# Performance work log

Hardware: AMD Instinct MI355X
Metric: run time of the kernel (lower is better)

Reference implementation:

```python
import jax, jax.numpy as jnp
import numpy as np

NGRAM = 3  # no_repeat_ngram_size from init_kwargs


def setup_inputs() -> dict:
    key = jax.random.key(0)
    k1, k2 = jax.random.split(key)
    B = 64 * 8          # bsz * beam_size
    L = 512             # step + 1 tokens generated so far
    V = 50257           # vocab
    tokens = jax.random.randint(k1, (B, L), 0, 50, dtype=jnp.int64)
    lprobs = jax.random.normal(k2, (B, V), dtype=jnp.float32)
    return {"tokens": tokens, "lprobs": lprobs, "bsz": 64, "beam_size": 8, "step": 511}


def _ngram_block(tokens, lprobs, step, n):
    """Vectorized equivalent of NGramRepeatBlock._no_repeat_ngram.

    For each row, the last n-1 tokens form the ngram prefix; any earlier
    position i in [0, step+2-n) whose (n-1)-gram matches it bans the token
    that followed it (tokens[i + n - 1]).
    """
    B, L = tokens.shape
    check = step + 2 - n  # number of start positions to check (static)
    if check <= 0:
        return lprobs
    # sliding (n-1)-gram windows at starts 0..check-1: (B, check, n-1)
    win_idx = jnp.arange(check)[:, None] + jnp.arange(n - 1)[None, :]
    windows = tokens[:, win_idx]
    prefix = tokens[:, L - (n - 1):]                    # (B, n-1) last n-1 tokens
    match = jnp.all(windows == prefix[:, None, :], -1)  # (B, check)
    banned_ids = tokens[:, n - 1: n - 1 + check]        # token following each window
    rows = jnp.arange(B)[:, None]
    banned = jnp.zeros(lprobs.shape, bool).at[rows, banned_ids].max(match)
    return jnp.where(banned, -jnp.inf, lprobs)


def reference(tokens, lprobs, bsz, beam_size, step):
    assert tokens.shape[0] == bsz * beam_size
    assert lprobs.shape[0] == bsz * beam_size
    return _ngram_block(tokens, lprobs, step, NGRAM)
```

## Files before the change

kernel.cpp:

```cpp
#include <hip/hip_runtime.h>

#define NGRAM 3
#define BAN_VALUE (-1.0e30f)

typedef float f32x4 __attribute__((ext_vector_type(4)));

#define UNROLL 4
#define TPB 256
#define BLK_F4 (TPB * UNROLL)

__global__ void __launch_bounds__(TPB)
copy_kernel(const float* __restrict__ in, float* __restrict__ out,
            long long n4) {
    const long long base = (long long)blockIdx.x * BLK_F4 + threadIdx.x;
    const f32x4* in4 = (const f32x4*)in;
    f32x4* out4 = (f32x4*)out;

    if (base + 3 * TPB < n4) {
        f32x4 v0 = __builtin_nontemporal_load(in4 + base);
        f32x4 v1 = __builtin_nontemporal_load(in4 + base + TPB);
        f32x4 v2 = __builtin_nontemporal_load(in4 + base + 2 * TPB);
        f32x4 v3 = __builtin_nontemporal_load(in4 + base + 3 * TPB);
        __builtin_nontemporal_store(v0, out4 + base);
        __builtin_nontemporal_store(v1, out4 + base + TPB);
        __builtin_nontemporal_store(v2, out4 + base + 2 * TPB);
        __builtin_nontemporal_store(v3, out4 + base + 3 * TPB);
    } else {
        for (int k = 0; k < UNROLL; ++k) {
            long long i = base + (long long)k * TPB;
            if (i < n4) {
                f32x4 v = __builtin_nontemporal_load(in4 + i);
                __builtin_nontemporal_store(v, out4 + i);
            }
        }
    }
}

__global__ void __launch_bounds__(TPB)
ban_kernel(const int* __restrict__ tokens, float* __restrict__ out,
           const int* __restrict__ step_p, int L, int V) {
    const int row = blockIdx.x;
    const int step = *step_p;
    const int check = step + 2 - NGRAM;
    if (check <= 0) return;

    const int* t = tokens + (long long)row * L;
    const int p0 = t[L - 2];
    const int p1 = t[L - 1];
    float* orow = out + (long long)row * V;

    for (int i = threadIdx.x; i < check; i += TPB) {
        if (t[i] == p0 && t[i + 1] == p1) {
            orow[t[i + 2]] = BAN_VALUE;
        }
    }
}

extern "C" void kernel_launch(void* const* d_in, const int* in_sizes, int n_in,
                              void* d_out, int out_size, void* d_ws, size_t ws_size,
                              hipStream_t stream) {
    const int*   tokens = (const int*)d_in[0];
    const float* lprobs = (const float*)d_in[1];
    const int*   step_p = (const int*)d_in[4];
    float*       out    = (float*)d_out;

    const int L = 512;
    const int B = in_sizes[0] / L;
    const int V = in_sizes[1] / B;
    const long long n = (long long)in_sizes[1];
    const long long n4 = n / 4;

    const int blocksA = (int)((n4 + BLK_F4 - 1) / BLK_F4);
    copy_kernel<<<blocksA, TPB, 0, stream>>>(lprobs, out, n4);

    ban_kernel<<<B, TPB, 0, stream>>>(tokens, out, step_p, L, V);
}
```

Before: 182.8 us.

## Fuse n-gram ban scatter into the streaming copy kernel

Merges the copy and ban kernels into one. Each copy block scans the token rows overlapping its slice, collects banned offsets in shared memory, and patches them into registers before the store. This removes the second launch and its scattered writes to global memory. In exchange, every block rescans full token rows (about 511 positions for one or two rows) and pays a per-block loop over the ban list, adding redundant token reads and compute to a bandwidth-bound copy.

```diff
diff --git a/kernel.cpp b/kernel.cpp
--- a/kernel.cpp
+++ b/kernel.cpp
@@ -8,51 +8,96 @@
 #define UNROLL 4
 #define TPB 256
 #define BLK_F4 (TPB * UNROLL)
+#define BLK_F  (BLK_F4 * 4)
+
+__device__ __forceinline__ f32x4 patch4(f32x4 v, int lane) {
+    v.x = (lane == 0) ? BAN_VALUE : v.x;
+    v.y = (lane == 1) ? BAN_VALUE : v.y;
+    v.z = (lane == 2) ? BAN_VALUE : v.z;
+    v.w = (lane == 3) ? BAN_VALUE : v.w;
+    return v;
+}
 
 __global__ void __launch_bounds__(TPB)
-copy_kernel(const float* __restrict__ in, float* __restrict__ out,
-            long long n4) {
-    const long long base = (long long)blockIdx.x * BLK_F4 + threadIdx.x;
+fused_kernel(const float* __restrict__ in, float* __restrict__ out,
+             const int* __restrict__ tokens, const int* __restrict__ step_p,
+             int L, int V, unsigned n_f)
+{
+    __shared__ int s_count;
+    __shared__ unsigned short s_list[1024];
+
+    const unsigned n4 = n_f >> 2;
+    const long long blk0 = (long long)blockIdx.x * BLK_F4;
+    const unsigned F0 = (unsigned)(blk0 * 4);
+    unsigned F1 = F0 + BLK_F; if (F1 > n_f) F1 = n_f;
+    const long long base = blk0 + threadIdx.x;
+    const bool blk_full = (blk0 + BLK_F4 <= (long long)n4);
+
+    if (threadIdx.x == 0) s_count = 0;
+    __syncthreads();
+
     const f32x4* in4 = (const f32x4*)in;
     f32x4* out4 = (f32x4*)out;
 
-    if (base + 3 * TPB < n4) {
-        f32x4 v0 = __builtin_nontemporal_load(in4 + base);
-        f32x4 v1 = __builtin_nontemporal_load(in4 + base + TPB);
-        f32x4 v2 = __builtin_nontemporal_load(in4 + base + 2 * TPB);
-        f32x4 v3 = __builtin_nontemporal_load(in4 + base + 3 * TPB);
+    f32x4 v0 = {}, v1 = {}, v2 = {}, v3 = {};
+    if (blk_full) {
+        v0 = __builtin_nontemporal_load(in4 + base);
+        v1 = __builtin_nontemporal_load(in4 + base + TPB);
+        v2 = __builtin_nontemporal_load(in4 + base + 2 * TPB);
+        v3 = __builtin_nontemporal_load(in4 + base + 3 * TPB);
+    } else {
+        if (base           < n4) v0 = __builtin_nontemporal_load(in4 + base);
+        if (base +     TPB < n4) v1 = __builtin_nontemporal_load(in4 + base + TPB);
+        if (base + 2 * TPB < n4) v2 = __builtin_nontemporal_load(in4 + base + 2 * TPB);
+        if (base + 3 * TPB < n4) v3 = __builtin_nontemporal_load(in4 + base + 3 * TPB);
+    }
+
+    const int step = *step_p;
+    const int check = step + 2 - NGRAM;
+    if (check > 0) {
+        const unsigned rlo = F0 / (unsigned)V;
+        const unsigned rhi = (F1 - 1) / (unsigned)V;
+        for (unsigned r = rlo; r <= rhi; ++r) {
+            const int* t = tokens + (long long)r * L;
+            const int p0 = t[L - 2];
+            const int p1 = t[L - 1];
+            for (int i = threadIdx.x; i < check; i += TPB) {
+                if (t[i] == p0 && t[i + 1] == p1) {
+                    const unsigned f = r * (unsigned)V + (unsigned)t[i + 2];
+                    if (f >= F0 && f < F1) {
+                        const int idx = atomicAdd(&s_count, 1);
+                        s_list[idx] = (unsigned short)(f - F0);
+                    }
+                }
+            }
+        }
+    }
+    __syncthreads();
+
+    const int cnt = s_count;
+    if (cnt > 0) {
+        const int tid = (int)threadIdx.x;
+        for (int j = 0; j < cnt; ++j) {
+            const int off  = (int)s_list[j];
+            const int q4   = off >> 2;
+            const int lane = off & 3;
+            if      (q4 == tid)            v0 = patch4(v0, lane);
+            else if (q4 == tid + TPB)      v1 = patch4(v1, lane);
+            else if (q4 == tid + 2 * TPB)  v2 = patch4(v2, lane);
+            else if (q4 == tid + 3 * TPB)  v3 = patch4(v3, lane);
+        }
+    }
+
+    if (blk_full) {
         __builtin_nontemporal_store(v0, out4 + base);
         __builtin_nontemporal_store(v1, out4 + base + TPB);
         __builtin_nontemporal_store(v2, out4 + base + 2 * TPB);
         __builtin_nontemporal_store(v3, out4 + base + 3 * TPB);
     } else {
-        for (int k = 0; k < UNROLL; ++k) {
-            long long i = base + (long long)k * TPB;
-            if (i < n4) {
-                f32x4 v = __builtin_nontemporal_load(in4 + i);
-                __builtin_nontemporal_store(v, out4 + i);
-            }
-        }
-    }
-}
-
-__global__ void __launch_bounds__(TPB)
-ban_kernel(const int* __restrict__ tokens, float* __restrict__ out,
-           const int* __restrict__ step_p, int L, int V) {
-    const int row = blockIdx.x;
-    const int step = *step_p;
-    const int check = step + 2 - NGRAM;
-    if (check <= 0) return;
-
-    const int* t = tokens + (long long)row * L;
-    const int p0 = t[L - 2];
-    const int p1 = t[L - 1];
-    float* orow = out + (long long)row * V;
-
-    for (int i = threadIdx.x; i < check; i += TPB) {
-        if (t[i] == p0 && t[i + 1] == p1) {
-            orow[t[i + 2]] = BAN_VALUE;
-        }
+        if (base           < n4) __builtin_nontemporal_store(v0, out4 + base);
+        if (base +     TPB < n4) __builtin_nontemporal_store(v1, out4 + base + TPB);
+        if (base + 2 * TPB < n4) __builtin_nontemporal_store(v2, out4 + base + 2 * TPB);
+        if (base + 3 * TPB < n4) __builtin_nontemporal_store(v3, out4 + base + 3 * TPB);
     }
 }
 
@@ -67,11 +112,9 @@
     const int L = 512;
     const int B = in_sizes[0] / L;
     const int V = in_sizes[1] / B;
-    const long long n = (long long)in_sizes[1];
-    const long long n4 = n / 4;
+    const unsigned n = (unsigned)in_sizes[1];
+    const unsigned n4 = n / 4;
 
-    const int blocksA = (int)((n4 + BLK_F4 - 1) / BLK_F4);
-    copy_kernel<<<blocksA, TPB, 0, stream>>>(lprobs, out, n4);
-
-    ban_kernel<<<B, TPB, 0, stream>>>(tokens, out, step_p, L, V);
+    const int blocks = (int)((n4 + BLK_F4 - 1) / BLK_F4);
+    fused_kernel<<<blocks, TPB, 0, stream>>>(lprobs, out, tokens, step_p, L, V, n);
 }
```

Measured after the change: 183.2 us. Within noise of the previous version (+0.2%).
